# Performance work log

Hardware: AMD Instinct MI355X
Metric: run time of the kernel (lower is better)

The kernel has to match this reference:

```python
import jax, jax.numpy as jnp
import numpy as np

N = 16384      # total nodes (hits)
K = 8          # n_neighbors
NB = 8         # number of graphs in batch
IN_C = 6       # in_channels
HID = 128      # hidden_channels
NCLS = 3       # num_classes
SLOPE = 0.2    # GATv2 leaky_relu negative_slope
BIG = 1e30     # mask value for cross-graph pairs


def setup_inputs() -> dict:
    key = jax.random.key(0)
    ks = jax.random.split(key, 32)
    coord = jax.random.normal(ks[0], (N, 3), dtype=jnp.float32)
    feat = jax.random.normal(ks[1], (N, IN_C), dtype=jnp.float32)
    batch = jnp.sort(jax.random.randint(ks[2], (N,), 0, NB)).astype(jnp.int32)

    def lin_w(k, fan_in, fan_out):
        return (jax.random.normal(k, (fan_in, fan_out), dtype=jnp.float32)
                * np.float32(1.0 / np.sqrt(fan_in)))

    inp = {"coord": coord, "feat": feat, "batch": batch}
    dims = [IN_C, HID, HID]  # input dim of each of the 3 GATv2 layers
    kidx = 3
    for l, din in enumerate(dims):
        inp[f"Wl{l}"] = lin_w(ks[kidx], din, HID); kidx += 1
        inp[f"bl{l}"] = jnp.zeros((HID,), jnp.float32)
        inp[f"Wr{l}"] = lin_w(ks[kidx], din, HID); kidx += 1
        inp[f"br{l}"] = jnp.zeros((HID,), jnp.float32)
        inp[f"att{l}"] = (jax.random.normal(ks[kidx], (HID,), dtype=jnp.float32)
                          * np.float32(1.0 / np.sqrt(HID))); kidx += 1
        inp[f"bias{l}"] = jnp.zeros((HID,), jnp.float32)
    inp["Wf"] = lin_w(ks[kidx], HID, NCLS)
    inp["bf"] = jnp.zeros((NCLS,), jnp.float32)
    return inp


def knn_idx(coord, batch):
    # pairwise squared distances, masked so neighbors stay within the same graph
    d2 = jnp.sum((coord[:, None, :] - coord[None, :, :]) ** 2, axis=-1)  # [N,N]
    d2 = jnp.where(batch[:, None] == batch[None, :], d2, BIG)
    _, idx = jax.lax.top_k(-d2, K)  # [N,K] nearest (includes self at dist 0)
    return idx


def gatv2_layer(x, idx, Wl, bl, Wr, br, att, bias):
    xl = x @ Wl + bl                         # [N,H] source transform
    xr = x @ Wr + br                         # [N,H] target transform
    g = xl[idx]                              # [N,K,H] gather neighbor features
    e = jax.nn.leaky_relu(g + xr[:, None, :], SLOPE)
    logits = e @ att                         # [N,K] attention scores
    alpha = jax.nn.softmax(logits, axis=1)   # softmax over each node's K nbrs
    return jnp.einsum('nk,nkh->nh', alpha, g) + bias


def reference(coord, feat, batch,
              Wl0, bl0, Wr0, br0, att0, bias0,
              Wl1, bl1, Wr1, br1, att1, bias1,
              Wl2, bl2, Wr2, br2, att2, bias2,
              Wf, bf):
    idx = knn_idx(coord, batch)
    x = jax.nn.relu(gatv2_layer(feat, idx, Wl0, bl0, Wr0, br0, att0, bias0))
    x = jax.nn.relu(gatv2_layer(x, idx, Wl1, bl1, Wr1, br1, att1, bias1))
    x = jax.nn.relu(gatv2_layer(x, idx, Wl2, bl2, Wr2, br2, att2, bias2))
    return x @ Wf + bf
```

## Files before the change

kernel.cpp:

```cpp
#include <hip/hip_runtime.h>
#include <hip/hip_bf16.h>
#include <float.h>
#include <limits.h>

#define NNODES 16384
#define KNB 8
#define HIDC 128
#define KNN_CAP 2560

__device__ __forceinline__ unsigned int dpp_shr1_u32(unsigned int v) {
  return (unsigned int)__builtin_amdgcn_update_dpp(0, (int)v, 0x111, 0xF, 0xF, true);
}
__device__ __forceinline__ float wave_sum(float x) {
  x += __int_as_float(__builtin_amdgcn_update_dpp(0, __float_as_int(x), 0xB1, 0xF, 0xF, true));
  x += __int_as_float(__builtin_amdgcn_update_dpp(0, __float_as_int(x), 0x4E, 0xF, 0xF, true));
  x += __int_as_float(__builtin_amdgcn_update_dpp(0, __float_as_int(x), 0x124, 0xF, 0xF, true));
  x += __int_as_float(__builtin_amdgcn_update_dpp(0, __float_as_int(x), 0x128, 0xF, 0xF, true));
  float r0 = __int_as_float(__builtin_amdgcn_readlane(__float_as_int(x), 0));
  float r1 = __int_as_float(__builtin_amdgcn_readlane(__float_as_int(x), 16));
  float r2 = __int_as_float(__builtin_amdgcn_readlane(__float_as_int(x), 32));
  float r3 = __int_as_float(__builtin_amdgcn_readlane(__float_as_int(x), 48));
  return (r0 + r1) + (r2 + r3);
}

__global__ __launch_bounds__(512) void knn_kernel(
    const float* __restrict__ coord, const int* __restrict__ batch,
    int* __restrict__ knn) {
  __shared__ float4 tile[KNN_CAP];
  int t = threadIdx.x;
  int lane = t & 63;
  int n0 = blockIdx.x * 8;
  int n = n0 + (t >> 6);

  int b0 = batch[n0], b7 = batch[n0 + 7], bw = batch[n];
  int lo = 0, hi = NNODES;
  while (lo < hi) { int m = (lo + hi) >> 1; if (batch[m] < b0) lo = m + 1; else hi = m; }
  int smin = lo;
  lo = n0 + 7; hi = NNODES;
  while (lo < hi) { int m = (lo + hi) >> 1; if (batch[m] <= b7) lo = m + 1; else hi = m; }
  int emax = lo;
  int s_w = smin, e_w = emax;
  if (bw != b0) {
    lo = n0; hi = NNODES;
    while (lo < hi) { int m = (lo + hi) >> 1; if (batch[m] < bw) lo = m + 1; else hi = m; }
    s_w = lo;
  }
  if (bw != b7) {
    lo = n; hi = NNODES;
    while (lo < hi) { int m = (lo + hi) >> 1; if (batch[m] <= bw) lo = m + 1; else hi = m; }
    e_w = lo;
  }
  int win_end = min(emax, smin + KNN_CAP);
  int cnt = win_end - smin;

  for (int i = t; i < cnt; i += 512) {
    const float* cp = coord + (size_t)(smin + i) * 3;
    tile[i] = make_float4(cp[0], cp[1], cp[2], 0.f);
  }
  __syncthreads();

  float cx = coord[n*3+0], cy = coord[n*3+1], cz = coord[n*3+2];

  unsigned long long tau = ~0ull;
  unsigned int llo = 0xFFFFFFFFu, lhi = 0xFFFFFFFFu;

  int lo_i = s_w - smin;
  int hi_i = min(e_w, win_end) - smin;
  for (int base = lo_i; base < hi_i; base += 64) {
    int i = base + lane;
    bool ok = i < hi_i;
    int ic = ok ? i : lo_i;
    float4 c = tile[ic];
    float dx = __fsub_rn(c.x, cx);
    float dy = __fsub_rn(c.y, cy);
    float dz = __fsub_rn(c.z, cz);
    float d = __fadd_rn(__fadd_rn(__fmul_rn(dx,dx), __fmul_rn(dy,dy)), __fmul_rn(dz,dz));
    unsigned long long ckey = ok
        ? (((unsigned long long)__float_as_uint(d) << 32) | (unsigned int)(smin + i))
        : ~0ull;
    unsigned long long m = __ballot(ckey < tau);
    if (m) {
      unsigned int c_lo = (unsigned int)ckey;
      unsigned int c_hi = (unsigned int)(ckey >> 32);
      do {
        int src = __builtin_ctzll(m);
        m &= m - 1;
        unsigned int nlo = (unsigned int)__builtin_amdgcn_readlane((int)c_lo, src);
        unsigned int nhi = (unsigned int)__builtin_amdgcn_readlane((int)c_hi, src);
        unsigned long long nk = ((unsigned long long)nhi << 32) | nlo;
        unsigned int plo = dpp_shr1_u32(llo);
        unsigned int phi = dpp_shr1_u32(lhi);
        unsigned long long pk = ((unsigned long long)phi << 32) | plo;
        unsigned long long ck = ((unsigned long long)lhi << 32) | llo;
        if (nk < ck) {
          unsigned long long r = (pk > nk) ? pk : nk;
          llo = (unsigned int)r; lhi = (unsigned int)(r >> 32);
        }
      } while (m);
      tau = (((unsigned long long)(unsigned int)__builtin_amdgcn_readlane((int)lhi, 7)) << 32)
            | (unsigned int)__builtin_amdgcn_readlane((int)llo, 7);
    }
  }
  for (int base = max(s_w, win_end); base < e_w; base += 64) {
    int j = base + lane;
    bool ok = j < e_w;
    int jc = ok ? j : s_w;
    float dx = __fsub_rn(coord[jc*3+0], cx);
    float dy = __fsub_rn(coord[jc*3+1], cy);
    float dz = __fsub_rn(coord[jc*3+2], cz);
    float d = __fadd_rn(__fadd_rn(__fmul_rn(dx,dx), __fmul_rn(dy,dy)), __fmul_rn(dz,dz));
    unsigned long long ckey = ok
        ? (((unsigned long long)__float_as_uint(d) << 32) | (unsigned int)j)
        : ~0ull;
    unsigned long long m = __ballot(ckey < tau);
    if (m) {
      unsigned int c_lo = (unsigned int)ckey;
      unsigned int c_hi = (unsigned int)(ckey >> 32);
      do {
        int src = __builtin_ctzll(m);
        m &= m - 1;
        unsigned int nlo = (unsigned int)__builtin_amdgcn_readlane((int)c_lo, src);
        unsigned int nhi = (unsigned int)__builtin_amdgcn_readlane((int)c_hi, src);
        unsigned long long nk = ((unsigned long long)nhi << 32) | nlo;
        unsigned int plo = dpp_shr1_u32(llo);
        unsigned int phi = dpp_shr1_u32(lhi);
        unsigned long long pk = ((unsigned long long)phi << 32) | plo;
        unsigned long long ck = ((unsigned long long)lhi << 32) | llo;
        if (nk < ck) {
          unsigned long long r = (pk > nk) ? pk : nk;
          llo = (unsigned int)r; lhi = (unsigned int)(r >> 32);
        }
      } while (m);
      tau = (((unsigned long long)(unsigned int)__builtin_amdgcn_readlane((int)lhi, 7)) << 32)
            | (unsigned int)__builtin_amdgcn_readlane((int)llo, 7);
    }
  }
  if (lane < KNB) knn[n*KNB + lane] = (int)llo;
}

template<int K>
__global__ __launch_bounds__(256) void lin2_kernel(
    const float* __restrict__ x,
    const float* __restrict__ Wl, const float* __restrict__ bl,
    const float* __restrict__ Wr, const float* __restrict__ br,
    float* __restrict__ xl, float* __restrict__ xr) {
  __shared__ float xs[32 * K];
  int t = threadIdx.x;
  int node0 = blockIdx.x * 32;
  for (int i = t; i < 32 * K; i += 256) xs[i] = x[node0 * K + i];
  __syncthreads();
  int cg = t & 63;
  int ng = t >> 6;
  int c0 = cg * 4;
  bool isR = (c0 >= HIDC);
  const float* W    = isR ? Wr : Wl;
  const float* bias = isR ? br : bl;
  float* dst        = isR ? xr : xl;
  int wc = isR ? (c0 - HIDC) : c0;

  float4 acc[8];
  #pragma unroll
  for (int nn = 0; nn < 8; ++nn) acc[nn] = make_float4(0.f, 0.f, 0.f, 0.f);

  if constexpr (K % 4 == 0) {
    for (int k0 = 0; k0 < K; k0 += 4) {
      float4 xv[8];
      #pragma unroll
      for (int nn = 0; nn < 8; ++nn)
        xv[nn] = *(const float4*)&xs[(ng * 8 + nn) * K + k0];
      #pragma unroll
      for (int q = 0; q < 4; ++q) {
        float4 w = *(const float4*)(W + (size_t)(k0 + q) * HIDC + wc);
        #pragma unroll
        for (int nn = 0; nn < 8; ++nn) {
          float xq = (q == 0) ? xv[nn].x : (q == 1) ? xv[nn].y : (q == 2) ? xv[nn].z : xv[nn].w;
          acc[nn].x = fmaf(xq, w.x, acc[nn].x);
          acc[nn].y = fmaf(xq, w.y, acc[nn].y);
          acc[nn].z = fmaf(xq, w.z, acc[nn].z);
          acc[nn].w = fmaf(xq, w.w, acc[nn].w);
        }
      }
    }
  } else {
    for (int k = 0; k < K; ++k) {
      float4 w = *(const float4*)(W + (size_t)k * HIDC + wc);
      #pragma unroll
      for (int nn = 0; nn < 8; ++nn) {
        float xq = xs[(ng * 8 + nn) * K + k];
        acc[nn].x = fmaf(xq, w.x, acc[nn].x);
        acc[nn].y = fmaf(xq, w.y, acc[nn].y);
        acc[nn].z = fmaf(xq, w.z, acc[nn].z);
        acc[nn].w = fmaf(xq, w.w, acc[nn].w);
      }
    }
  }
  float4 b4 = *(const float4*)(bias + wc);
  #pragma unroll
  for (int nn = 0; nn < 8; ++nn) {
    int node = node0 + ng * 8 + nn;
    float4 o;
    o.x = acc[nn].x + b4.x; o.y = acc[nn].y + b4.y;
    o.z = acc[nn].z + b4.z; o.w = acc[nn].w + b4.w;
    *(float4*)(dst + (size_t)node * HIDC + wc) = o;
  }
}

template<bool FINAL>
__global__ __launch_bounds__(256) void gat_attn_kernel(
    const float* __restrict__ xl, const float* __restrict__ xr,
    const int* __restrict__ knn, const float* __restrict__ att,
    const float* __restrict__ bias, float* __restrict__ xout,
    const float* __restrict__ Wf, const float* __restrict__ bf,
    float* __restrict__ out) {
  int wid = threadIdx.x >> 6;
  int lane = threadIdx.x & 63;
  int n = blockIdx.x * 4 + wid;
  int c0 = 2 * lane, c1 = 2 * lane + 1;
  float2 xr2 = *(const float2*)(xr + (size_t)n * HIDC + c0);
  float2 a2  = *(const float2*)(att + c0);
  int myj = (lane < KNB) ? knn[n * KNB + lane] : 0;
  float g0[8], g1[8], lg[8];
  #pragma unroll
  for (int k = 0; k < 8; ++k) {
    int j = __builtin_amdgcn_readlane(myj, k);
    float2 g = *(const float2*)(xl + (size_t)j * HIDC + c0);
    g0[k] = g.x; g1[k] = g.y;
    float e0 = g.x + xr2.x; e0 = (e0 > 0.f) ? e0 : 0.2f * e0;
    float e1 = g.y + xr2.y; e1 = (e1 > 0.f) ? e1 : 0.2f * e1;
    lg[k] = wave_sum(e0 * a2.x + e1 * a2.y);
  }
  float mx = lg[0];
  #pragma unroll
  for (int k = 1; k < 8; ++k) mx = fmaxf(mx, lg[k]);
  float ssum = 0.f, w[8];
  #pragma unroll
  for (int k = 0; k < 8; ++k) { w[k] = __expf(lg[k] - mx); ssum += w[k]; }
  float inv = 1.f / ssum;
  float o0 = 0.f, o1 = 0.f;
  #pragma unroll
  for (int k = 0; k < 8; ++k) { o0 += w[k] * g0[k]; o1 += w[k] * g1[k]; }
  o0 = fmaxf(fmaf(o0, inv, bias[c0]), 0.f);
  o1 = fmaxf(fmaf(o1, inv, bias[c1]), 0.f);
  if (!FINAL) {
    float2 o; o.x = o0; o.y = o1;
    *(float2*)(xout + (size_t)n * HIDC + c0) = o;
  } else {
    #pragma unroll
    for (int cls = 0; cls < 3; ++cls) {
      float p = wave_sum(o0 * Wf[c0 * 3 + cls] + o1 * Wf[c1 * 3 + cls]);
      if (lane == 0) out[n * 3 + cls] = p + bf[cls];
    }
  }
}

extern "C" void kernel_launch(void* const* d_in, const int* in_sizes, int n_in,
                              void* d_out, int out_size, void* d_ws, size_t ws_size,
                              hipStream_t stream) {
  const float* coord = (const float*)d_in[0];
  const float* feat  = (const float*)d_in[1];
  const int*   batch = (const int*)d_in[2];
  const float* Wl0 = (const float*)d_in[3];
  const float* bl0 = (const float*)d_in[4];
  const float* Wr0 = (const float*)d_in[5];
  const float* br0 = (const float*)d_in[6];
  const float* att0  = (const float*)d_in[7];
  const float* bias0 = (const float*)d_in[8];
  const float* Wl1 = (const float*)d_in[9];
  const float* bl1 = (const float*)d_in[10];
  const float* Wr1 = (const float*)d_in[11];
  const float* br1 = (const float*)d_in[12];
  const float* att1  = (const float*)d_in[13];
  const float* bias1 = (const float*)d_in[14];
  const float* Wl2 = (const float*)d_in[15];
  const float* bl2 = (const float*)d_in[16];
  const float* Wr2 = (const float*)d_in[17];
  const float* br2 = (const float*)d_in[18];
  const float* att2  = (const float*)d_in[19];
  const float* bias2 = (const float*)d_in[20];
  const float* Wf = (const float*)d_in[21];
  const float* bf = (const float*)d_in[22];
  float* out = (float*)d_out;

  char* ws = (char*)d_ws;
  int*   knn = (int*)ws;
  float* xl  = (float*)(ws + (512 << 10));
  float* xr  = xl + (size_t)NNODES * HIDC;
  float* xb0 = xr + (size_t)NNODES * HIDC;
  float* xb1 = xb0 + (size_t)NNODES * HIDC;

  knn_kernel<<<NNODES / 8, 512, 0, stream>>>(coord, batch, knn);

  lin2_kernel<6><<<NNODES / 32, 256, 0, stream>>>(feat, Wl0, bl0, Wr0, br0, xl, xr);
  gat_attn_kernel<false><<<NNODES / 4, 256, 0, stream>>>(xl, xr, knn, att0, bias0, xb0,
                                                         nullptr, nullptr, nullptr);

  lin2_kernel<128><<<NNODES / 32, 256, 0, stream>>>(xb0, Wl1, bl1, Wr1, br1, xl, xr);
  gat_attn_kernel<false><<<NNODES / 4, 256, 0, stream>>>(xl, xr, knn, att1, bias1, xb1,
                                                         nullptr, nullptr, nullptr);

  lin2_kernel<128><<<NNODES / 32, 256, 0, stream>>>(xb1, Wl2, bl2, Wr2, br2, xl, xr);
  gat_attn_kernel<true><<<NNODES / 4, 256, 0, stream>>>(xl, xr, knn, att2, bias2, nullptr,
                                                        Wf, bf, out);
}
```

Measured before the change: 166.7 us.

## Precompute graph segment bounds, prime kNN threshold early, batch tile scan by four

```diff
diff --git a/kernel.cpp b/kernel.cpp
--- a/kernel.cpp
+++ b/kernel.cpp
@@ -23,9 +23,40 @@
   return (r0 + r1) + (r2 + r3);
 }
 
+__device__ __forceinline__ void insert_survivors(
+    unsigned long long m, unsigned int c_lo, unsigned int c_hi,
+    unsigned int& llo, unsigned int& lhi, unsigned long long& tau) {
+  while (m) {
+    int src = __builtin_ctzll(m);
+    m &= m - 1;
+    unsigned int nlo = (unsigned int)__builtin_amdgcn_readlane((int)c_lo, src);
+    unsigned int nhi = (unsigned int)__builtin_amdgcn_readlane((int)c_hi, src);
+    unsigned long long nk = ((unsigned long long)nhi << 32) | nlo;
+    if (nk >= tau) continue;
+    unsigned int plo = dpp_shr1_u32(llo);
+    unsigned int phi = dpp_shr1_u32(lhi);
+    unsigned long long pk = ((unsigned long long)phi << 32) | plo;
+    unsigned long long ck = ((unsigned long long)lhi << 32) | llo;
+    if (nk < ck) {
+      unsigned long long r = (pk > nk) ? pk : nk;
+      llo = (unsigned int)r; lhi = (unsigned int)(r >> 32);
+    }
+    tau = (((unsigned long long)(unsigned int)__builtin_amdgcn_readlane((int)lhi, 7)) << 32)
+          | (unsigned int)__builtin_amdgcn_readlane((int)llo, 7);
+  }
+}
+
+__global__ void seg_kernel(const int* __restrict__ batch, int* __restrict__ seg) {
+  int b = threadIdx.x;
+  if (b > 8) return;
+  int lo = 0, hi = NNODES;
+  while (lo < hi) { int m = (lo + hi) >> 1; if (batch[m] < b) lo = m + 1; else hi = m; }
+  seg[b] = lo;
+}
+
 __global__ __launch_bounds__(512) void knn_kernel(
     const float* __restrict__ coord, const int* __restrict__ batch,
-    int* __restrict__ knn) {
+    const int* __restrict__ seg, int* __restrict__ knn) {
   __shared__ float4 tile[KNN_CAP];
   int t = threadIdx.x;
   int lane = t & 63;
@@ -33,23 +64,10 @@
   int n = n0 + (t >> 6);
 
   int b0 = batch[n0], b7 = batch[n0 + 7], bw = batch[n];
-  int lo = 0, hi = NNODES;
-  while (lo < hi) { int m = (lo + hi) >> 1; if (batch[m] < b0) lo = m + 1; else hi = m; }
-  int smin = lo;
-  lo = n0 + 7; hi = NNODES;
-  while (lo < hi) { int m = (lo + hi) >> 1; if (batch[m] <= b7) lo = m + 1; else hi = m; }
-  int emax = lo;
-  int s_w = smin, e_w = emax;
-  if (bw != b0) {
-    lo = n0; hi = NNODES;
-    while (lo < hi) { int m = (lo + hi) >> 1; if (batch[m] < bw) lo = m + 1; else hi = m; }
-    s_w = lo;
-  }
-  if (bw != b7) {
-    lo = n; hi = NNODES;
-    while (lo < hi) { int m = (lo + hi) >> 1; if (batch[m] <= bw) lo = m + 1; else hi = m; }
-    e_w = lo;
-  }
+  int smin = seg[b0];
+  int emax = seg[b7 + 1];
+  int s_w = seg[bw];
+  int e_w = seg[bw + 1];
   int win_end = min(emax, smin + KNN_CAP);
   int cnt = win_end - smin;
 
@@ -57,51 +75,51 @@
     const float* cp = coord + (size_t)(smin + i) * 3;
     tile[i] = make_float4(cp[0], cp[1], cp[2], 0.f);
   }
-  __syncthreads();
 
   float cx = coord[n*3+0], cy = coord[n*3+1], cz = coord[n*3+2];
 
   unsigned long long tau = ~0ull;
   unsigned int llo = 0xFFFFFFFFu, lhi = 0xFFFFFFFFu;
 
+  {
+    int j = s_w + lane;
+    bool ok = j < e_w;
+    int jc = ok ? j : s_w;
+    float dx = __fsub_rn(coord[jc*3+0], cx);
+    float dy = __fsub_rn(coord[jc*3+1], cy);
+    float dz = __fsub_rn(coord[jc*3+2], cz);
+    float d = __fadd_rn(__fadd_rn(__fmul_rn(dx,dx), __fmul_rn(dy,dy)), __fmul_rn(dz,dz));
+    unsigned int klo = (unsigned int)j;
+    unsigned int khi = __float_as_uint(d);
+    insert_survivors(__ballot(ok), klo, khi, llo, lhi, tau);
+  }
+
+  __syncthreads();
+
   int lo_i = s_w - smin;
   int hi_i = min(e_w, win_end) - smin;
-  for (int base = lo_i; base < hi_i; base += 64) {
-    int i = base + lane;
-    bool ok = i < hi_i;
-    int ic = ok ? i : lo_i;
-    float4 c = tile[ic];
-    float dx = __fsub_rn(c.x, cx);
-    float dy = __fsub_rn(c.y, cy);
-    float dz = __fsub_rn(c.z, cz);
-    float d = __fadd_rn(__fadd_rn(__fmul_rn(dx,dx), __fmul_rn(dy,dy)), __fmul_rn(dz,dz));
-    unsigned long long ckey = ok
-        ? (((unsigned long long)__float_as_uint(d) << 32) | (unsigned int)(smin + i))
-        : ~0ull;
-    unsigned long long m = __ballot(ckey < tau);
-    if (m) {
-      unsigned int c_lo = (unsigned int)ckey;
-      unsigned int c_hi = (unsigned int)(ckey >> 32);
-      do {
-        int src = __builtin_ctzll(m);
-        m &= m - 1;
-        unsigned int nlo = (unsigned int)__builtin_amdgcn_readlane((int)c_lo, src);
-        unsigned int nhi = (unsigned int)__builtin_amdgcn_readlane((int)c_hi, src);
-        unsigned long long nk = ((unsigned long long)nhi << 32) | nlo;
-        unsigned int plo = dpp_shr1_u32(llo);
-        unsigned int phi = dpp_shr1_u32(lhi);
-        unsigned long long pk = ((unsigned long long)phi << 32) | plo;
-        unsigned long long ck = ((unsigned long long)lhi << 32) | llo;
-        if (nk < ck) {
-          unsigned long long r = (pk > nk) ? pk : nk;
-          llo = (unsigned int)r; lhi = (unsigned int)(r >> 32);
-        }
-      } while (m);
-      tau = (((unsigned long long)(unsigned int)__builtin_amdgcn_readlane((int)lhi, 7)) << 32)
-            | (unsigned int)__builtin_amdgcn_readlane((int)llo, 7);
-    }
-  }
-  for (int base = max(s_w, win_end); base < e_w; base += 64) {
+  for (int base = lo_i + 64; base < hi_i; base += 256) {
+    unsigned long long k[4];
+    #pragma unroll
+    for (int q = 0; q < 4; ++q) {
+      int i = base + lane + 64 * q;
+      bool ok = i < hi_i;
+      float4 c = tile[ok ? i : 0];
+      float dx = __fsub_rn(c.x, cx);
+      float dy = __fsub_rn(c.y, cy);
+      float dz = __fsub_rn(c.z, cz);
+      float d = __fadd_rn(__fadd_rn(__fmul_rn(dx,dx), __fmul_rn(dy,dy)), __fmul_rn(dz,dz));
+      k[q] = ok ? (((unsigned long long)__float_as_uint(d) << 32) | (unsigned int)(smin + i))
+                : ~0ull;
+    }
+    #pragma unroll
+    for (int q = 0; q < 4; ++q) {
+      unsigned long long m = __ballot(k[q] < tau);
+      if (m) insert_survivors(m, (unsigned int)k[q], (unsigned int)(k[q] >> 32), llo, lhi, tau);
+    }
+  }
+
+  for (int base = max(s_w + 64, win_end); base < e_w; base += 64) {
     int j = base + lane;
     bool ok = j < e_w;
     int jc = ok ? j : s_w;
@@ -113,27 +131,7 @@
         ? (((unsigned long long)__float_as_uint(d) << 32) | (unsigned int)j)
         : ~0ull;
     unsigned long long m = __ballot(ckey < tau);
-    if (m) {
-      unsigned int c_lo = (unsigned int)ckey;
-      unsigned int c_hi = (unsigned int)(ckey >> 32);
-      do {
-        int src = __builtin_ctzll(m);
-        m &= m - 1;
-        unsigned int nlo = (unsigned int)__builtin_amdgcn_readlane((int)c_lo, src);
-        unsigned int nhi = (unsigned int)__builtin_amdgcn_readlane((int)c_hi, src);
-        unsigned long long nk = ((unsigned long long)nhi << 32) | nlo;
-        unsigned int plo = dpp_shr1_u32(llo);
-        unsigned int phi = dpp_shr1_u32(lhi);
-        unsigned long long pk = ((unsigned long long)phi << 32) | plo;
-        unsigned long long ck = ((unsigned long long)lhi << 32) | llo;
-        if (nk < ck) {
-          unsigned long long r = (pk > nk) ? pk : nk;
-          llo = (unsigned int)r; lhi = (unsigned int)(r >> 32);
-        }
-      } while (m);
-      tau = (((unsigned long long)(unsigned int)__builtin_amdgcn_readlane((int)lhi, 7)) << 32)
-            | (unsigned int)__builtin_amdgcn_readlane((int)llo, 7);
-    }
+    if (m) insert_survivors(m, (unsigned int)ckey, (unsigned int)(ckey >> 32), llo, lhi, tau);
   }
   if (lane < KNB) knn[n*KNB + lane] = (int)llo;
 }
@@ -287,8 +285,10 @@
   float* xr  = xl + (size_t)NNODES * HIDC;
   float* xb0 = xr + (size_t)NNODES * HIDC;
   float* xb1 = xb0 + (size_t)NNODES * HIDC;
-
-  knn_kernel<<<NNODES / 8, 512, 0, stream>>>(coord, batch, knn);
+  int*   seg = (int*)xb0;
+
+  seg_kernel<<<1, 16, 0, stream>>>(batch, seg);
+  knn_kernel<<<NNODES / 8, 512, 0, stream>>>(coord, batch, seg, knn);
 
   lin2_kernel<6><<<NNODES / 32, 256, 0, stream>>>(feat, Wl0, bl0, Wr0, br0, xl, xr);
   gat_attn_kernel<false><<<NNODES / 4, 256, 0, stream>>>(xl, xr, knn, att0, bias0, xb0,
```

New measurement: 167.6 us. About the same (+0.5%).
